# Optimization experiments

Measured on AMD Instinct MI355X. Metric: run time of the kernel, lower is better.

The kernel has to match this reference:

```python
import jax, jax.numpy as jnp
import numpy as np

BS, TS, NE, ED = 32, 64, 64, 96
E = 256        # attn_embed_dim
H = 4          # attn_n_heads
HD = E // H    # head dim
RNN_H = 256
N_ACT = 32
NA = 16        # n_agents


def setup_inputs():
    key = jax.random.key(0)
    ks = jax.random.split(key, 40)
    entities = jax.random.normal(ks[0], (BS, TS, NE, ED), jnp.float32)
    obs_mask = jax.random.randint(ks[1], (BS, TS, NE, NE), 0, 2).astype(jnp.float32)  # 1 = masked
    entity_mask = (jax.random.uniform(ks[2], (BS, TS, NE)) < 0.1).astype(jnp.float32)  # 1 = inactive
    hidden_state = jnp.zeros((BS * NA, RNN_H), jnp.float32)
    it = iter(range(3, 40))
    def lin(fi, fo):
        return jax.random.normal(ks[next(it)], (fi, fo), jnp.float32) / np.sqrt(fi).astype(np.float32)
    p = dict(
        fc1_w=lin(ED, E), fc1_b=jnp.zeros((E,), jnp.float32),
        attn_in_w=lin(E, 3 * E), attn_out_w=lin(E, E), attn_out_b=jnp.zeros((E,), jnp.float32),
        fc2_w=lin(2 * E, RNN_H), fc2_b=jnp.zeros((RNN_H,), jnp.float32),
        gru_w_ih=lin(RNN_H, 3 * RNN_H), gru_w_hh=lin(RNN_H, 3 * RNN_H),
        gru_b_ih=jnp.zeros((3 * RNN_H,), jnp.float32), gru_b_hh=jnp.zeros((3 * RNN_H,), jnp.float32),
        fc3_w=lin(RNN_H, N_ACT), fc3_b=jnp.zeros((N_ACT,), jnp.float32),
        fcmsg1_w=lin(ED, E), fcmsg1_b=jnp.zeros((E,), jnp.float32),
        lmsg_in_w=lin(E, 3 * E), lmsg_out_w=lin(E, E), lmsg_out_b=jnp.zeros((E,), jnp.float32),
        gmsg_in_w=lin(E, 3 * E), gmsg_out_w=lin(E, E), gmsg_out_b=jnp.zeros((E,), jnp.float32),
        gate_in_w=lin(E, 3 * E), gate_out_w=lin(E, E), gate_out_b=jnp.zeros((E,), jnp.float32),
        gatefc1_w=lin(ED, E), gatefc1_b=jnp.zeros((E,), jnp.float32),
        gatefc2_w=lin(E, 2), gatefc2_b=jnp.zeros((2,), jnp.float32),
    )
    return dict(entities=entities, obs_mask=obs_mask, entity_mask=entity_mask,
                hidden_state=hidden_state, **p)


def _attn(x, in_w, out_w, out_b, pre_mask, post_mask):
    """REFIL EntityAttentionLayer: n_queries = NA agent rows, masks use 1 = masked."""
    B, ne, e = x.shape
    q, k, v = jnp.split(x @ in_w, 3, axis=-1)                       # each [B, ne, E]
    q = q[:, :NA].reshape(B, NA, H, HD).transpose(0, 2, 1, 3)        # [B, H, NA, HD]
    k = k.reshape(B, ne, H, HD).transpose(0, 2, 1, 3)                # [B, H, ne, HD]
    v = v.reshape(B, ne, H, HD).transpose(0, 2, 1, 3)
    logits = jnp.einsum('bhqd,bhkd->bhqk', q, k) / jnp.asarray(np.sqrt(HD), x.dtype)
    m = pre_mask[:, None, :NA, :]                                    # [B, 1, NA, ne]
    logits = jnp.where(m > 0, jnp.asarray(-1e9, x.dtype), logits)
    # softmax; zeroing masked cols also reproduces torch's NaN->0 for fully-masked rows
    w = jax.nn.softmax(logits, axis=-1) * (1.0 - m)
    out = jnp.einsum('bhqk,bhkd->bhqd', w, v).transpose(0, 2, 1, 3).reshape(B, NA, e)
    out = out @ out_w + out_b
    return out * (1.0 - post_mask[..., None])                        # masked_fill(post_mask, 0)


def _forward(entities, obs_mask, entity_mask, hidden_state,
             fc1_w, fc1_b, attn_in_w, attn_out_w, attn_out_b, fc2_w, fc2_b,
             gru_w_ih, gru_w_hh, gru_b_ih, gru_b_hh, fc3_w, fc3_b,
             fcmsg1_w, fcmsg1_b, lmsg_in_w, lmsg_out_w, lmsg_out_b,
             gmsg_in_w, gmsg_out_w, gmsg_out_b, gate_in_w, gate_out_w, gate_out_b,
             gatefc1_w, gatefc1_b, gatefc2_w, gatefc2_b):
    bs, ts, ne, ed = entities.shape
    B = bs * ts
    ent = entities.reshape(B, ne, ed)
    om = obs_mask.reshape(B, ne, ne)
    em = entity_mask.reshape(B, ne)
    agent_mask = em[:, :NA]                                          # [B, NA]
    full_obs_mask = 1.0 - (1.0 - agent_mask[:, None, :]) * (1.0 - agent_mask[:, :, None])

    x1 = jax.nn.relu(ent @ fc1_w + fc1_b)
    x2 = _attn(x1, attn_in_w, attn_out_w, attn_out_b, om, agent_mask)          # [B, NA, E]

    x1_msg = jax.nn.relu(ent @ fcmsg1_w + fcmsg1_b)
    x1_gate = jax.nn.relu(ent @ gatefc1_w + gatefc1_b)
    x2_msg = _attn(x1_msg, lmsg_in_w, lmsg_out_w, lmsg_out_b, om, agent_mask)  # [B, NA, E]
    x2_gate = _attn(x1_gate, gate_in_w, gate_out_w, gate_out_b, om, agent_mask)
    x2_gate = x2_gate @ gatefc2_w + gatefc2_b                                   # [B, NA, 2]

    # argmax of softmax == argmax of logits; gate in {0,1}, non-differentiable
    gate = jnp.argmax(x2_gate, axis=-1).astype(entities.dtype)
    gated_msg = x2_msg * gate[..., None]
    global_msg = _attn(gated_msg, gmsg_in_w, gmsg_out_w, gmsg_out_b,
                       full_obs_mask, agent_mask)                               # [B, NA, E]

    x3 = jax.nn.relu(jnp.concatenate([x2, global_msg], axis=-1) @ fc2_w + fc2_b)
    x3 = x3.reshape(bs, ts, NA, RNN_H)

    # GRU recurrence over ts via scan; hidden flattened to [bs*NA, RNN_H]
    h0 = hidden_state.reshape(-1, RNN_H)
    xs = x3.transpose(1, 0, 2, 3).reshape(ts, bs * NA, RNN_H)

    def step(h, x):
        gi = x @ gru_w_ih + gru_b_ih
        gh = h @ gru_w_hh + gru_b_hh
        ir, iz, inn = jnp.split(gi, 3, axis=-1)
        hr, hz, hn = jnp.split(gh, 3, axis=-1)
        r = jax.nn.sigmoid(ir + hr)
        z = jax.nn.sigmoid(iz + hz)
        n = jnp.tanh(inn + r * hn)
        h_new = (1.0 - z) * n + z * h
        return h_new, h_new

    _, hs = jax.lax.scan(step, h0, xs)                               # [ts, bs*NA, RNN_H]
    hs = hs.reshape(ts, bs, NA, RNN_H).transpose(1, 0, 2, 3)         # [bs, ts, NA, RNN_H]

    q = hs @ fc3_w + fc3_b                                           # [bs, ts, NA, N_ACT]
    am = agent_mask.reshape(bs, ts, NA, 1)
    q = q * (1.0 - am)                                               # masked_fill(agent_mask, 0)
    return q, hs, x2_gate


def reference(entities, obs_mask, entity_mask, hidden_state,
              fc1_w, fc1_b, attn_in_w, attn_out_w, attn_out_b, fc2_w, fc2_b,
              gru_w_ih, gru_w_hh, gru_b_ih, gru_b_hh, fc3_w, fc3_b,
              fcmsg1_w, fcmsg1_b, lmsg_in_w, lmsg_out_w, lmsg_out_b,
              gmsg_in_w, gmsg_out_w, gmsg_out_b, gate_in_w, gate_out_w, gate_out_b,
              gatefc1_w, gatefc1_b, gatefc2_w, gatefc2_b):
    return _forward(entities, obs_mask, entity_mask, hidden_state,
                    fc1_w, fc1_b, attn_in_w, attn_out_w, attn_out_b, fc2_w, fc2_b,
                    gru_w_ih, gru_w_hh, gru_b_ih, gru_b_hh, fc3_w, fc3_b,
                    fcmsg1_w, fcmsg1_b, lmsg_in_w, lmsg_out_w, lmsg_out_b,
                    gmsg_in_w, gmsg_out_w, gmsg_out_b, gate_in_w, gate_out_w, gate_out_b,
                    gatefc1_w, gatefc1_b, gatefc2_w, gatefc2_b)
```

## Files before the change

kernel.cpp:

```cpp
#include <hip/hip_runtime.h>


#define DEV __device__ __forceinline__

typedef _Float16 f16x8 __attribute__((ext_vector_type(8)));
typedef _Float16 f16x4 __attribute__((ext_vector_type(4)));
typedef float    f32x4 __attribute__((ext_vector_type(4)));
typedef float    f32x16 __attribute__((ext_vector_type(16)));

DEV f32x4 mfma16(f16x8 a, f16x8 b, f32x4 c){
  return __builtin_amdgcn_mfma_f32_16x16x32_f16(a, b, c, 0, 0, 0);
}
DEV f32x16 mfma32(f16x8 a, f16x8 b, f32x16 c){
  return __builtin_amdgcn_mfma_f32_32x32x16_f16(a, b, c, 0, 0, 0);
}

template<int MODE> struct AB {
  f16x8 hi, lo;
  DEV void mf(const AB& b, f32x4& c) const {
    if constexpr (MODE){
      c = mfma16(lo, b.hi, c);
      c = mfma16(hi, b.lo, c);
    }
    c = mfma16(hi, b.hi, c);
  }
};

template<int MODE> DEV AB<MODE> ldW(const _Float16* p, int losz){
  AB<MODE> r; r.hi = *(const f16x8*)p;
  if constexpr (MODE) r.lo = *(const f16x8*)(p + losz);
  return r;
}
template<int MODE> DEV AB<MODE> ldL(const _Float16* ph, const _Float16* pl){
  AB<MODE> r; r.hi = *(const f16x8*)ph;
  if constexpr (MODE) r.lo = *(const f16x8*)pl;
  return r;
}
template<int MODE> DEV AB<MODE> ldF(const float* p){
  AB<MODE> r;
  f32x4 v0 = *(const f32x4*)p, v1 = *(const f32x4*)(p + 4);
#pragma unroll
  for (int i = 0; i < 4; ++i){
    float a = v0[i], b = v1[i];
    _Float16 ah = (_Float16)a, bh = (_Float16)b;
    r.hi[i] = ah; r.hi[i+4] = bh;
    if constexpr (MODE){
      r.lo[i]   = (_Float16)(a - (float)ah);
      r.lo[i+4] = (_Float16)(b - (float)bh);
    }
  }
  return r;
}
template<int MODE> DEV void stL(_Float16* ph, _Float16* pl, int idx, float v){
  _Float16 h = (_Float16)v;
  ph[idx] = h;
  if constexpr (MODE) pl[idx] = (_Float16)(v - (float)h);
}

struct WJobs {
  const float* src[15];
  unsigned off[15];
  int K[15], N[15], mode[15];
};

__global__ __launch_bounds__(256) void k0_conv(WJobs jb, char* ws){
  const int job = blockIdx.y;
  const int K = jb.K[job], N = jb.N[job];
  const int total = K * N;
  _Float16* dh = (_Float16*)(ws + jb.off[job]);
  const float* src = jb.src[job];
  const int m = jb.mode[job];
  for (int idx = blockIdx.x*256 + threadIdx.x; idx < total; idx += gridDim.x*256){
    int n = idx / K, k = idx - n*K;
    float v = src[(size_t)k*N + n];
    _Float16 h = (_Float16)v;
    dh[idx] = h;
    if (m) dh[total + idx] = (_Float16)(v - (float)h);
  }
}

__global__ __launch_bounds__(256) void k0w_gate(
    const float* __restrict__ Wout, const float* __restrict__ Wg2,
    const float* __restrict__ bo,   const float* __restrict__ Win,
    _Float16* __restrict__ wveff, float* __restrict__ beff)
{
  __shared__ float weff_s[256*2];
  const int tid = threadIdx.x;
  {
    float a0 = 0.f, a1 = 0.f;
    const float* wr = Wout + (size_t)tid*256;
    for (int f = 0; f < 256; ++f){ float x = wr[f]; a0 += x*Wg2[2*f]; a1 += x*Wg2[2*f+1]; }
    weff_s[tid*2] = a0; weff_s[tid*2+1] = a1;
  }
  if (tid < 2){
    float s = 0.f;
    for (int f = 0; f < 256; ++f) s += bo[f]*Wg2[2*f + tid];
    beff[tid] = s;
  }
  __syncthreads();
  {
    const int j = tid;
    for (int n = 0; n < 16; ++n){
      float v = 0.f;
      if (n < 8){
        int h = n >> 1, c = n & 1;
        const float* wr = Win + (size_t)j*768 + 512 + h*64;
        const float* we = weff_s + (h*64)*2 + c;
        for (int d = 0; d < 64; ++d) v += wr[d]*we[2*d];
      }
      _Float16 hi = (_Float16)v;
      wveff[n*256 + j] = hi;
      wveff[16*256 + n*256 + j] = (_Float16)(v - (float)hi);
    }
  }
}

__global__ __launch_bounds__(512) void k1_all(
    const float* __restrict__ ent, const float* __restrict__ om, const float* __restrict__ em,
    const _Float16* __restrict__ W1a, const float* __restrict__ b1a,
    const _Float16* __restrict__ WINa,
    const _Float16* __restrict__ WOUTa, const float* __restrict__ boa,
    float* __restrict__ x2outa,
    const _Float16* __restrict__ W1b, const float* __restrict__ b1b,
    const _Float16* __restrict__ WINb,
    const _Float16* __restrict__ WOUTb, const float* __restrict__ bob,
    float* __restrict__ x2outb,
    const _Float16* __restrict__ W1g, const float* __restrict__ b1g,
    const _Float16* __restrict__ WINg,
    const _Float16* __restrict__ WVEFF,
    const float* __restrict__ beff, const float* __restrict__ gb2,
    float* __restrict__ og, float* __restrict__ gate)
{
  const int tid = threadIdx.x;
  const int w = tid >> 6, lg = (tid >> 4) & 3, li = tid & 15;
  extern __shared__ char smem[];

  if (blockIdx.x < 2048){
    const int br = blockIdx.x >> 10;
    const int p  = blockIdx.x & 1023;
    const int bb2[2] = { 2*p, 2*p + 1 };
    const _Float16* W1   = br ? W1b   : W1a;
    const float*    b1   = br ? b1b   : b1a;
    const _Float16* WIN  = br ? WINb  : WINa;
    const _Float16* WOUT = br ? WOUTb : WOUTa;
    const float*    bo   = br ? bob   : boa;
    float*          x2out= br ? x2outb: x2outa;

    const int wi = w & 3, ih = w >> 2;
    const int l = tid & 63;
    const int r32 = l & 31, kh = (l >> 5)*8;

    _Float16* x1   = (_Float16*)smem;
    _Float16* Ks   = (_Float16*)(smem + 67584);
    _Float16* Vs   = (_Float16*)(smem + 86016);
    _Float16* Qful = (_Float16*)(smem + 104448);
    float*    lgs  = (float*)(smem + 121344);
    _Float16* Ps   = (_Float16*)(smem + 130560);
    _Float16* outp = (_Float16*)(smem + 135168);

    {
      const int b = bb2[ih];
      _Float16* x1p = x1 + ih*16896;
      const int mt = wi & 1, ntb = (wi >> 1)*4;
      f32x16 acc0 = 0.f, acc1 = 0.f, acc2 = 0.f, acc3 = 0.f;
#pragma unroll
      for (int kk = 0; kk < 6; ++kk){
        AB<0> a = ldF<0>(ent + ((size_t)b*64 + mt*32 + r32)*96 + kk*16 + kh);
        f16x8 B0 = *(const f16x8*)(W1 + (size_t)((ntb + 0)*32 + r32)*96 + kk*16 + kh);
        f16x8 B1 = *(const f16x8*)(W1 + (size_t)((ntb + 1)*32 + r32)*96 + kk*16 + kh);
        f16x8 B2 = *(const f16x8*)(W1 + (size_t)((ntb + 2)*32 + r32)*96 + kk*16 + kh);
        f16x8 B3 = *(const f16x8*)(W1 + (size_t)((ntb + 3)*32 + r32)*96 + kk*16 + kh);
        acc0 = mfma32(a.hi, B0, acc0);
        acc1 = mfma32(a.hi, B1, acc1);
        acc2 = mfma32(a.hi, B2, acc2);
        acc3 = mfma32(a.hi, B3, acc3);
      }
#pragma unroll
      for (int s = 0; s < 4; ++s){
        const f32x16& ac = (s == 0) ? acc0 : (s == 1) ? acc1 : (s == 2) ? acc2 : acc3;
        int col = (ntb + s)*32 + r32;
        float bias = b1[col];
#pragma unroll
        for (int reg = 0; reg < 16; ++reg){
          int row = (reg & 3) + 8*(reg >> 2) + 4*(l >> 5);
          x1p[(mt*32 + row)*264 + col] = (_Float16)fmaxf(ac[reg] + bias, 0.f);
        }
      }
    }
    __syncthreads();

    {
      f32x16 acc = 0.f;
      const int itq = r32 >> 4, qr = r32 & 15;
      for (int kk = 0; kk < 16; ++kk){
        f16x8 A = *(const f16x8*)(x1 + itq*16896 + qr*264 + kk*16 + kh);
        f16x8 B = *(const f16x8*)(WIN + (size_t)(w*32 + r32)*256 + kk*16 + kh);
        acc = mfma32(A, B, acc);
      }
#pragma unroll
      for (int reg = 0; reg < 16; ++reg){
        int row = (reg & 3) + 8*(reg >> 2) + 4*(l >> 5);
        Qful[(row >> 4)*4224 + (row & 15)*264 + w*32 + r32] = (_Float16)acc[reg];
      }
    }
    __syncthreads();

    for (int h = 0; h < 4; ++h){
      if (w < 4){
        const int kt = w >> 1, dt = w & 1;
        f32x16 acc0 = 0.f, acc1 = 0.f;
        for (int kk = 0; kk < 16; ++kk){
          int ao = (kt*32 + r32)*264 + kk*16 + kh;
          f16x8 A0 = *(const f16x8*)(x1 + ao);
          f16x8 A1 = *(const f16x8*)(x1 + 16896 + ao);
          f16x8 B = *(const f16x8*)(WIN + (size_t)(256 + 64*h + dt*32 + r32)*256 + kk*16 + kh);
          acc0 = mfma32(A0, B, acc0);
          acc1 = mfma32(A1, B, acc1);
        }
#pragma unroll
        for (int reg = 0; reg < 16; ++reg){
          int row = (reg & 3) + 8*(reg >> 2) + 4*(l >> 5);
          Ks[(kt*32 + row)*72 + dt*32 + r32]        = (_Float16)acc0[reg];
          Ks[4608 + (kt*32 + row)*72 + dt*32 + r32] = (_Float16)acc1[reg];
        }
      } else {
        const int wv = w - 4;
        const int kt = wv >> 1, dt = wv & 1;
        f32x16 acc0 = 0.f, acc1 = 0.f;
        for (int kk = 0; kk < 16; ++kk){
          int ao = (kt*32 + r32)*264 + kk*16 + kh;
          f16x8 A0 = *(const f16x8*)(x1 + ao);
          f16x8 A1 = *(const f16x8*)(x1 + 16896 + ao);
          f16x8 B = *(const f16x8*)(WIN + (size_t)(512 + 64*h + dt*32 + r32)*256 + kk*16 + kh);
          acc0 = mfma32(A0, B, acc0);
          acc1 = mfma32(A1, B, acc1);
        }
#pragma unroll
        for (int rr = 0; rr < 4; ++rr){
          f16x4 p0, p1;
#pragma unroll
          for (int q4 = 0; q4 < 4; ++q4){
            p0[q4] = (_Float16)acc0[rr*4 + q4];
            p1[q4] = (_Float16)acc1[rr*4 + q4];
          }
          int key = kt*32 + rr*8 + 4*(l >> 5);
          *(f16x4*)(Vs + (dt*32 + r32)*72 + key)        = p0;
          *(f16x4*)(Vs + 4608 + (dt*32 + r32)*72 + key) = p1;
        }
      }
      __syncthreads();
      {
        const int b = bb2[ih];
        f32x4 acc = 0.f;
#pragma unroll
        for (int kk = 0; kk < 2; ++kk){
          f16x8 A = *(const f16x8*)(Qful + ih*4224 + li*264 + 64*h + kk*32 + lg*8);
          f16x8 B = *(const f16x8*)(Ks + ih*4608 + (16*wi + li)*72 + kk*32 + lg*8);
          acc = mfma16(A, B, acc);
        }
#pragma unroll
        for (int j = 0; j < 4; ++j){
          int q = 4*lg + j, key = 16*wi + li;
          float v = acc[j] * 0.125f;
          float m = om[((size_t)b*64 + q)*64 + key];
          if (m > 0.f) v = -1e9f;
          lgs[ih*1152 + q*72 + key] = v;
        }
      }
      __syncthreads();
      {
        const int it = tid >> 8, q = (tid >> 4) & 15, i16 = tid & 15;
        const int b = bb2[it];
        float pv[4], mx = -3e38f;
#pragma unroll
        for (int u = 0; u < 4; ++u){ pv[u] = lgs[it*1152 + q*72 + i16 + 16*u]; mx = fmaxf(mx, pv[u]); }
#pragma unroll
        for (int d = 1; d < 16; d <<= 1) mx = fmaxf(mx, __shfl_xor(mx, d, 16));
        float s = 0.f;
#pragma unroll
        for (int u = 0; u < 4; ++u){ pv[u] = expf(pv[u] - mx); s += pv[u]; }
#pragma unroll
        for (int d = 1; d < 16; d <<= 1) s += __shfl_xor(s, d, 16);
#pragma unroll
        for (int u = 0; u < 4; ++u){
          int key = i16 + 16*u;
          float m = om[((size_t)b*64 + q)*64 + key];
          Ps[it*1152 + q*72 + key] = (_Float16)((pv[u]/s)*(1.f - m));
        }
      }
      __syncthreads();
      {
        f32x4 acc = 0.f;
#pragma unroll
        for (int kk = 0; kk < 2; ++kk){
          f16x8 A = *(const f16x8*)(Ps + ih*1152 + li*72 + kk*32 + lg*8);
          f16x8 B = *(const f16x8*)(Vs + ih*4608 + (16*wi + li)*72 + kk*32 + lg*8);
          acc = mfma16(A, B, acc);
        }
#pragma unroll
        for (int j = 0; j < 4; ++j)
          outp[ih*4224 + (4*lg + j)*264 + 64*h + 16*wi + li] = (_Float16)acc[j];
      }
      __syncthreads();
    }

    {
      f32x16 acc = 0.f;
      const int ito = r32 >> 4, qr = r32 & 15;
      for (int kk = 0; kk < 16; ++kk){
        f16x8 A = *(const f16x8*)(outp + ito*4224 + qr*264 + kk*16 + kh);
        f16x8 B = *(const f16x8*)(WOUT + (size_t)(w*32 + r32)*256 + kk*16 + kh);
        acc = mfma32(A, B, acc);
      }
      int col = w*32 + r32;
      float bias = bo[col];
#pragma unroll
      for (int reg = 0; reg < 16; ++reg){
        int row = (reg & 3) + 8*(reg >> 2) + 4*(l >> 5);
        int it2 = row >> 4, q2 = row & 15;
        const int b = bb2[it2];
        float v = (acc[reg] + bias) * (1.f - em[(size_t)b*64 + q2]);
        x2out[((size_t)b*16 + q2)*256 + col] = v;
      }
    }
    return;
  }

  {
    constexpr int W1SZ = 96*256, WINSZ = 256*768, WVSZ = 16*256;
    const int b = blockIdx.x - 2048;
    const int l = tid & 63;
    const int r32 = l & 31, kh = (l >> 5)*8;

    char* sp = smem;
    _Float16* x1h = (_Float16*)sp; sp += 64*264*2;
    _Float16* x1l = (_Float16*)sp; sp += 64*264*2;
    _Float16* Kh  = (_Float16*)sp; sp += 64*72*2;
    _Float16* Kl  = (_Float16*)sp; sp += 64*72*2;
    _Float16* Qh  = (_Float16*)sp; sp += 16*264*2;
    _Float16* Ql  = (_Float16*)sp; sp += 16*264*2;
    float*    lgs = (float*)sp;    sp += 16*72*4;
    float*    Ps  = (float*)sp;    sp += 16*66*4;
    float*    v2s = (float*)sp;    sp += 64*18*4;
    float*  ogacc = (float*)sp;    sp += 32*4;
    float*  Kpart = (float*)sp;    sp += 8192*4;

    {
      const int mt = w & 1, ntb = (w >> 1)*2;
      f32x16 acc0 = 0.f, acc1 = 0.f;
#pragma unroll
      for (int kk = 0; kk < 6; ++kk){
        AB<1> a = ldF<1>(ent + ((size_t)b*64 + mt*32 + r32)*96 + kk*16 + kh);
#pragma unroll
        for (int s = 0; s < 2; ++s){
          const _Float16* bp = W1g + (size_t)((ntb + s)*32 + r32)*96 + kk*16 + kh;
          f16x8 Bh = *(const f16x8*)bp;
          f16x8 Bl = *(const f16x8*)(bp + W1SZ);
          f32x16& ac = s ? acc1 : acc0;
          ac = mfma32(a.lo, Bh, ac);
          ac = mfma32(a.hi, Bl, ac);
          ac = mfma32(a.hi, Bh, ac);
        }
      }
#pragma unroll
      for (int s = 0; s < 2; ++s){
        const f32x16& ac = s ? acc1 : acc0;
        int col = (ntb + s)*32 + r32;
        float bias = b1g[col];
#pragma unroll
        for (int reg = 0; reg < 16; ++reg){
          int row = (reg & 3) + 8*(reg >> 2) + 4*(l >> 5);
          stL<1>(x1h, x1l, (mt*32 + row)*264 + col, fmaxf(ac[reg] + bias, 0.f));
        }
      }
    }
    if (tid < 32) ogacc[tid] = 0.f;
    __syncthreads();

    {
#pragma unroll
      for (int s = 0; s < 2; ++s){
        int nt = w + s*8;
        f32x4 acc = 0.f;
        for (int kk = 0; kk < 8; ++kk){
          int ao = li*264 + kk*32 + lg*8;
          AB<1> a = ldL<1>(x1h + ao, x1l + ao);
          AB<1> bb = ldW<1>(WINg + (size_t)(nt*16 + li)*256 + kk*32 + lg*8, WINSZ);
          a.mf(bb, acc);
        }
#pragma unroll
        for (int j = 0; j < 4; ++j)
          stL<1>(Qh, Ql, (4*lg + j)*264 + nt*16 + li, acc[j]);
      }
      if (w < 4){
        f32x4 acc = 0.f;
        for (int kk = 0; kk < 8; ++kk){
          int ao = (w*16 + li)*264 + kk*32 + lg*8;
          AB<1> a = ldL<1>(x1h + ao, x1l + ao);
          AB<1> bb = ldW<1>(WVEFF + (size_t)li*256 + kk*32 + lg*8, WVSZ);
          a.mf(bb, acc);
        }
#pragma unroll
        for (int j = 0; j < 4; ++j)
          v2s[(w*16 + 4*lg + j)*18 + li] = acc[j];
      }
    }
    __syncthreads();

    for (int h = 0; h < 4; ++h){
      {
        const int t = w & 3, kt = t >> 1, dt = t & 1, khalf = w >> 2;
        f32x16 acc = 0.f;
#pragma unroll
        for (int k8 = 0; k8 < 8; ++k8){
          int ko = (khalf*8 + k8)*16 + kh;
          int ao = (kt*32 + r32)*264 + ko;
          f16x8 ah = *(const f16x8*)(x1h + ao);
          f16x8 al = *(const f16x8*)(x1l + ao);
          const _Float16* bp = WINg + (size_t)(256 + h*64 + dt*32 + r32)*256 + ko;
          f16x8 Bh = *(const f16x8*)bp;
          f16x8 Bl = *(const f16x8*)(bp + WINSZ);
          acc = mfma32(al, Bh, acc);
          acc = mfma32(ah, Bl, acc);
          acc = mfma32(ah, Bh, acc);
        }
#pragma unroll
        for (int reg = 0; reg < 16; ++reg){
          int row = (reg & 3) + 8*(reg >> 2) + 4*(l >> 5);
          Kpart[((khalf*4 + t)*32 + row)*32 + r32] = acc[reg];
        }
      }
      __syncthreads();
      {
        for (int e = tid; e < 4096; e += 512){
          float s2 = Kpart[e] + Kpart[4096 + e];
          int t2 = e >> 10, idx = e & 1023, row = idx >> 5, col = idx & 31;
          stL<1>(Kh, Kl, ((t2 >> 1)*32 + row)*72 + (t2 & 1)*32 + col, s2);
        }
      }
      __syncthreads();
      if (w < 4){
        f32x4 acc = 0.f;
#pragma unroll
        for (int kk = 0; kk < 2; ++kk){
          int ao = li*264 + h*64 + kk*32 + lg*8;
          AB<1> a = ldL<1>(Qh + ao, Ql + ao);
          int bo_ = (16*w + li)*72 + kk*32 + lg*8;
          AB<1> bb = ldL<1>(Kh + bo_, Kl + bo_);
          a.mf(bb, acc);
        }
#pragma unroll
        for (int j = 0; j < 4; ++j){
          int q = 4*lg + j, key = 16*w + li;
          float v = acc[j] * 0.125f;
          float m = om[((size_t)b*64 + q)*64 + key];
          if (m > 0.f) v = -1e9f;
          lgs[q*72 + key] = v;
        }
      }
      __syncthreads();
      if (tid < 256){
        int q = tid >> 4, i16 = tid & 15;
        float pv[4], mx = -3e38f;
#pragma unroll
        for (int u = 0; u < 4; ++u){ pv[u] = lgs[q*72 + i16 + 16*u]; mx = fmaxf(mx, pv[u]); }
#pragma unroll
        for (int d = 1; d < 16; d <<= 1) mx = fmaxf(mx, __shfl_xor(mx, d, 16));
        float s = 0.f;
#pragma unroll
        for (int u = 0; u < 4; ++u){ pv[u] = expf(pv[u] - mx); s += pv[u]; }
#pragma unroll
        for (int d = 1; d < 16; d <<= 1) s += __shfl_xor(s, d, 16);
#pragma unroll
        for (int u = 0; u < 4; ++u){
          int key = i16 + 16*u;
          float m = om[((size_t)b*64 + q)*64 + key];
          Ps[q*66 + key] = (pv[u]/s)*(1.f - m);
        }
      }
      __syncthreads();
      if (tid < 256){
        int q = tid >> 4, l16 = tid & 15;
        float a0 = 0.f, a1 = 0.f;
#pragma unroll
        for (int u = 0; u < 4; ++u){
          int k = l16 + 16*u;
          float p2 = Ps[q*66 + k];
          a0 += p2 * v2s[k*18 + h*2];
          a1 += p2 * v2s[k*18 + h*2 + 1];
        }
#pragma unroll
        for (int d = 1; d < 16; d <<= 1){ a0 += __shfl_xor(a0, d, 16); a1 += __shfl_xor(a1, d, 16); }
        if (l16 == 0){ ogacc[q*2] += a0; ogacc[q*2 + 1] += a1; }
      }
      __syncthreads();
    }
    if (tid < 16){
      int q = tid;
      float am = em[(size_t)b*64 + q];
      float g0 = (1.f - am)*(ogacc[2*q]     + beff[0]) + gb2[0];
      float g1 = (1.f - am)*(ogacc[2*q + 1] + beff[1]) + gb2[1];
      og[((size_t)b*16 + q)*2]     = g0;
      og[((size_t)b*16 + q)*2 + 1] = g1;
      gate[(size_t)b*16 + q] = (g1 > g0) ? 1.f : 0.f;
    }
  }
}

__global__ __launch_bounds__(256) void k2_global(
    const float* __restrict__ em,
    const float* __restrict__ x2, const float* __restrict__ x2m,
    const float* __restrict__ gate,
    const _Float16* __restrict__ GMIN, const _Float16* __restrict__ GMOUT, const float* __restrict__ gob,
    const _Float16* __restrict__ FC2T, const float* __restrict__ fc2b,
    const _Float16* __restrict__ GIHT, const float* __restrict__ gib,
    float* __restrict__ gi)
{
  const int p = blockIdx.x;
  const int tid = threadIdx.x;
  const int w = tid >> 6, lg = (tid >> 4) & 3, li = tid & 15;

  extern __shared__ char smem[];
  float*    gate_s = (float*)smem;
  _Float16* gm_s   = (_Float16*)(smem + 128);
  _Float16* Q2     = (_Float16*)(smem + 17024);
  _Float16* K2s    = (_Float16*)(smem + 21632);
  _Float16* Vt2    = (_Float16*)(smem + 26240);
  float*    lg2    = (float*)(smem + 36480);
  _Float16* P2     = (_Float16*)(smem + 39552);
  _Float16* outp   = (_Float16*)(smem + 42112);
  _Float16* cat_s  = (_Float16*)(smem + 59008);
  _Float16* x3_s   = (_Float16*)(smem + 92288);

  if (tid < 32){
    int it = tid >> 4, q = tid & 15;
    gate_s[it*16 + q] = gate[(size_t)(2*p + it)*16 + q];
  }
  __syncthreads();
#pragma unroll
  for (int it = 0; it < 2; ++it){
    const int b = 2*p + it;
    for (int idx = tid; idx < 4096; idx += 256){
      int q = idx >> 8, d = idx & 255;
      gm_s[it*4224 + q*264 + d]  = (_Float16)(x2m[((size_t)b*16 + q)*256 + d] * gate_s[it*16 + q]);
      cat_s[it*8320 + q*520 + d] = (_Float16)(x2[((size_t)b*16 + q)*256 + d]);
    }
  }
  for (int idx = tid; idx < 2*64*40; idx += 256) Vt2[idx] = (_Float16)0.f;
  for (int idx = tid; idx < 2*16*40; idx += 256) P2[idx] = (_Float16)0.f;
  __syncthreads();
  for (int h = 0; h < 4; ++h){
    {
      f32x4 aq0 = 0.f, aq1 = 0.f, ak0 = 0.f, ak1 = 0.f, av0 = 0.f, av1 = 0.f;
      for (int kk = 0; kk < 8; ++kk){
        f16x8 A0 = *(const f16x8*)(gm_s + li*264 + kk*32 + lg*8);
        f16x8 A1 = *(const f16x8*)(gm_s + 4224 + li*264 + kk*32 + lg*8);
        f16x8 Bq = *(const f16x8*)(GMIN + (size_t)(      64*h + 16*w + li)*256 + kk*32 + lg*8);
        f16x8 Bk = *(const f16x8*)(GMIN + (size_t)(256 + 64*h + 16*w + li)*256 + kk*32 + lg*8);
        f16x8 Bv = *(const f16x8*)(GMIN + (size_t)(512 + 64*h + 16*w + li)*256 + kk*32 + lg*8);
        aq0 = mfma16(A0, Bq, aq0); aq1 = mfma16(A1, Bq, aq1);
        ak0 = mfma16(A0, Bk, ak0); ak1 = mfma16(A1, Bk, ak1);
        av0 = mfma16(A0, Bv, av0); av1 = mfma16(A1, Bv, av1);
      }
#pragma unroll
      for (int j = 0; j < 4; ++j){
        int rw = 4*lg + j, dim = 16*w + li;
        Q2[rw*72 + dim]         = (_Float16)aq0[j];
        Q2[1152 + rw*72 + dim]  = (_Float16)aq1[j];
        K2s[rw*72 + dim]        = (_Float16)ak0[j];
        K2s[1152 + rw*72 + dim] = (_Float16)ak1[j];
        Vt2[dim*40 + rw]        = (_Float16)av0[j];
        Vt2[2560 + dim*40 + rw] = (_Float16)av1[j];
      }
    }
    __syncthreads();
    if (w < 2){
      const int it = w, b = 2*p + it;
      f32x4 acc = 0.f;
#pragma unroll
      for (int kk = 0; kk < 2; ++kk){
        f16x8 A = *(const f16x8*)(Q2  + it*1152 + li*72 + kk*32 + lg*8);
        f16x8 B = *(const f16x8*)(K2s + it*1152 + li*72 + kk*32 + lg*8);
        acc = mfma16(A, B, acc);
      }
      float amk = em[(size_t)b*64 + li];
#pragma unroll
      for (int j = 0; j < 4; ++j){
        int q = 4*lg + j;
        float amq = em[(size_t)b*64 + q];
        float m = 1.f - (1.f - amq)*(1.f - amk);
        float v = acc[j]*0.125f;
        if (m > 0.f) v = -1e9f;
        lg2[it*384 + q*24 + li] = v;
      }
    }
    __syncthreads();
    {
      int q = tid >> 4, key = tid & 15;
#pragma unroll
      for (int it = 0; it < 2; ++it){
        const int b = 2*p + it;
        float v = lg2[it*384 + q*24 + key];
        float mx = v;
#pragma unroll
        for (int d = 1; d < 16; d <<= 1) mx = fmaxf(mx, __shfl_xor(mx, d, 16));
        float pe = expf(v - mx);
        float s = pe;
#pragma unroll
        for (int d = 1; d < 16; d <<= 1) s += __shfl_xor(s, d, 16);
        float amq = em[(size_t)b*64 + q], amk = em[(size_t)b*64 + key];
        float m = 1.f - (1.f - amq)*(1.f - amk);
        P2[it*640 + q*40 + key] = (_Float16)((pe/s)*(1.f - m));
      }
    }
    __syncthreads();
    {
#pragma unroll
      for (int it = 0; it < 2; ++it){
        f32x4 acc = 0.f;
        f16x8 A = *(const f16x8*)(P2 + it*640 + li*40 + lg*8);
        f16x8 B = *(const f16x8*)(Vt2 + it*2560 + (16*w + li)*40 + lg*8);
        acc = mfma16(A, B, acc);
#pragma unroll
        for (int j = 0; j < 4; ++j)
          outp[it*4224 + (4*lg + j)*264 + 64*h + 16*w + li] = (_Float16)acc[j];
      }
    }
    __syncthreads();
  }
  {
#pragma unroll
    for (int c = 0; c < 4; ++c){
      int col = 64*w + 16*c + li;
      f32x4 a0 = 0.f, a1 = 0.f;
      for (int kk = 0; kk < 8; ++kk){
        f16x8 B  = *(const f16x8*)(GMOUT + (size_t)col*256 + kk*32 + lg*8);
        f16x8 A0 = *(const f16x8*)(outp + li*264 + kk*32 + lg*8);
        f16x8 A1 = *(const f16x8*)(outp + 4224 + li*264 + kk*32 + lg*8);
        a0 = mfma16(A0, B, a0);
        a1 = mfma16(A1, B, a1);
      }
      float bias = gob[col];
#pragma unroll
      for (int j = 0; j < 4; ++j){
        int q = 4*lg + j;
        float m0 = 1.f - em[(size_t)(2*p)*64 + q];
        float m1 = 1.f - em[(size_t)(2*p + 1)*64 + q];
        cat_s[q*520 + 256 + col]        = (_Float16)((a0[j] + bias)*m0);
        cat_s[8320 + q*520 + 256 + col] = (_Float16)((a1[j] + bias)*m1);
      }
    }
  }
  __syncthreads();
  {
#pragma unroll
    for (int c = 0; c < 4; ++c){
      int col = 64*w + 16*c + li;
      f32x4 a0 = 0.f, a1 = 0.f;
      for (int kk = 0; kk < 16; ++kk){
        f16x8 B  = *(const f16x8*)(FC2T + (size_t)col*512 + kk*32 + lg*8);
        f16x8 A0 = *(const f16x8*)(cat_s + li*520 + kk*32 + lg*8);
        f16x8 A1 = *(const f16x8*)(cat_s + 8320 + li*520 + kk*32 + lg*8);
        a0 = mfma16(A0, B, a0);
        a1 = mfma16(A1, B, a1);
      }
      float bias = fc2b[col];
#pragma unroll
      for (int j = 0; j < 4; ++j){
        x3_s[(4*lg + j)*264 + col]        = (_Float16)fmaxf(a0[j] + bias, 0.f);
        x3_s[4224 + (4*lg + j)*264 + col] = (_Float16)fmaxf(a1[j] + bias, 0.f);
      }
    }
  }
  __syncthreads();
  {
    const int r0 = ((2*p) >> 6)*16, t0 = (2*p) & 63;
#pragma unroll
    for (int cc = 0; cc < 12; ++cc){
      int col = (w*12 + cc)*16 + li;
      f32x4 a0 = 0.f, a1 = 0.f;
      for (int kk = 0; kk < 8; ++kk){
        f16x8 B  = *(const f16x8*)(GIHT + (size_t)col*256 + kk*32 + lg*8);
        f16x8 A0 = *(const f16x8*)(x3_s + li*264 + kk*32 + lg*8);
        f16x8 A1 = *(const f16x8*)(x3_s + 4224 + li*264 + kk*32 + lg*8);
        a0 = mfma16(A0, B, a0);
        a1 = mfma16(A1, B, a1);
      }
      float bias = gib[col];
#pragma unroll
      for (int j = 0; j < 4; ++j){
        int q = 4*lg + j;
        gi[((size_t)((r0 + q)*64 + t0))*768 + col]     = a0[j] + bias;
        gi[((size_t)((r0 + q)*64 + t0 + 1))*768 + col] = a1[j] + bias;
      }
    }
  }
}

__global__ __launch_bounds__(256) void k3_gru(
    const _Float16* __restrict__ WHH, const float* __restrict__ bhh,
    const float* __restrict__ gi, const float* __restrict__ h0,
    float* __restrict__ hs)
{
  const int rb = blockIdx.x;
  const int row0 = rb * 16;
  const int tid = threadIdx.x;
  const int w = tid >> 6, lg = (tid >> 4) & 3, li = tid & 15;

  extern __shared__ char smem3[];
  _Float16* hf16 = (_Float16*)smem3;
  float* hf32 = (float*)(smem3 + 8448);
  float* gh   = (float*)(smem3 + 8448 + 16640);
  float* bhs  = (float*)(smem3 + 8448 + 16640 + 49664);

  for (int idx = tid; idx < 768; idx += 256) bhs[idx] = bhh[idx];
  for (int idx = tid; idx < 4096; idx += 256){
    int r = idx >> 8, d = idx & 255;
    float v = h0[(size_t)(row0 + r)*256 + d];
    hf32[r*260 + d] = v;
    hf16[r*264 + d] = (_Float16)v;
  }
  __syncthreads();

  const int er = tid >> 4;
  const int d0 = (tid & 15) * 16;

  for (int t = 0; t < 64; ++t){
    const float* gp = gi + ((size_t)(row0 + er)*64 + t)*768 + d0;
    f32x4 gr[4], gz[4], gn[4];
#pragma unroll
    for (int v = 0; v < 4; ++v){
      gr[v] = *(const f32x4*)(gp + v*4);
      gz[v] = *(const f32x4*)(gp + 256 + v*4);
      gn[v] = *(const f32x4*)(gp + 512 + v*4);
    }
    f16x8 a[8];
#pragma unroll
    for (int kk = 0; kk < 8; ++kk)
      a[kk] = *(const f16x8*)(hf16 + li*264 + kk*32 + lg*8);
    f32x4 acc[12];
#pragma unroll
    for (int c = 0; c < 12; ++c) acc[c] = 0.f;
#pragma unroll
    for (int c = 0; c < 12; ++c){
      const _Float16* bp = WHH + (size_t)(w*192 + c*16 + li)*256 + lg*8;
#pragma unroll
      for (int kk = 0; kk < 8; ++kk)
        acc[c] = mfma16(a[kk], *(const f16x8*)(bp + kk*32), acc[c]);
    }
#pragma unroll
    for (int c = 0; c < 12; ++c){
      int col = w*192 + c*16 + li;
#pragma unroll
      for (int j = 0; j < 4; ++j)
        gh[(4*lg + j)*776 + col] = acc[c][j];
    }
    __syncthreads();
    {
      float* hp32 = hf32 + er*260 + d0;
      float* hsp  = hs + ((size_t)(rb*64 + t)*16 + er)*256 + d0;
      f16x8 hv8[2];
#pragma unroll
      for (int v = 0; v < 4; ++v){
        f32x4 xr = *(const f32x4*)(gh + er*776 +       d0 + v*4);
        f32x4 xz = *(const f32x4*)(gh + er*776 + 256 + d0 + v*4);
        f32x4 xn = *(const f32x4*)(gh + er*776 + 512 + d0 + v*4);
        f32x4 hold = *(const f32x4*)(hp32 + v*4);
        f32x4 hout;
#pragma unroll
        for (int e = 0; e < 4; ++e){
          int d = d0 + v*4 + e;
          float rr_ = 1.f/(1.f + __expf(-(gr[v][e] + xr[e] + bhs[d])));
          float zz  = 1.f/(1.f + __expf(-(gz[v][e] + xz[e] + bhs[256 + d])));
          float pre = gn[v][e] + rr_*(xn[e] + bhs[512 + d]);
          float nn  = 1.f - 2.f/(1.f + __expf(2.f*pre));
          float hv = (1.f - zz)*nn + zz*hold[e];
          hout[e] = hv;
          int sl = v*4 + e;
          hv8[sl >> 3][sl & 7] = (_Float16)hv;
        }
        *(f32x4*)(hp32 + v*4) = hout;
        *(f32x4*)(hsp + v*4)  = hout;
      }
      *(f16x8*)(hf16 + er*264 + d0)     = hv8[0];
      *(f16x8*)(hf16 + er*264 + d0 + 8) = hv8[1];
    }
    __syncthreads();
  }
}

__global__ __launch_bounds__(256) void k4_q(
    const _Float16* __restrict__ FC3T, const float* __restrict__ fc3b,
    const float* __restrict__ em, const float* __restrict__ hs, float* __restrict__ qo)
{
  const int tid = threadIdx.x;
  const int w = tid >> 6, lg = (tid >> 4) & 3, li = tid & 15;
  const int rb = blockIdx.x*64 + 16*w;
  f32x4 acc[2];
#pragma unroll
  for (int c = 0; c < 2; ++c) acc[c] = 0.f;
  for (int kk = 0; kk < 8; ++kk){
    const float* ap = hs + (size_t)(rb + li)*256 + kk*32 + lg*8;
    f32x4 v0 = *(const f32x4*)ap, v1 = *(const f32x4*)(ap + 4);
    f16x8 A;
#pragma unroll
    for (int e = 0; e < 4; ++e){ A[e] = (_Float16)v0[e]; A[e+4] = (_Float16)v1[e]; }
#pragma unroll
    for (int c = 0; c < 2; ++c){
      f16x8 B = *(const f16x8*)(FC3T + (size_t)(16*c + li)*256 + kk*32 + lg*8);
      acc[c] = mfma16(A, B, acc[c]);
    }
  }
#pragma unroll
  for (int c = 0; c < 2; ++c){
    int col = 16*c + li;
    float bias = fc3b[col];
#pragma unroll
    for (int j = 0; j < 4; ++j){
      int row = rb + 4*lg + j;
      float am = em[(size_t)(row >> 4)*64 + (row & 15)];
      qo[(size_t)row*32 + col] = (acc[c][j] + bias)*(1.f - am);
    }
  }
}

extern "C" void kernel_launch(void* const* d_in, const int* in_sizes, int n_in,
                              void* d_out, int out_size, void* d_ws, size_t ws_size,
                              hipStream_t stream)
{
  constexpr size_t OFF_FC1T   = 0;
  constexpr size_t OFF_MSG1T  = 49152;
  constexpr size_t OFF_AINT   = 98304;
  constexpr size_t OFF_LINT   = 491520;
  constexpr size_t OFF_AOUTT  = 884736;
  constexpr size_t OFF_LOUTT  = 1015808;
  constexpr size_t OFF_GMINT  = 1146880;
  constexpr size_t OFF_GMOUTT = 1540096;
  constexpr size_t OFF_FC2T   = 1671168;
  constexpr size_t OFF_GIHT   = 1933312;
  constexpr size_t OFF_GHHT   = 2326528;
  constexpr size_t OFF_FC3T   = 2719744;
  constexpr size_t OFF_G1T    = 2736128;
  constexpr size_t OFF_GINT   = 2834432;
  constexpr size_t OFF_WVEFF  = 3620864;
  constexpr size_t OFF_BEFF   = 3637248;
  constexpr size_t OFF_GATE   = 3637504;
  constexpr size_t OFF_X2     = 3768576;
  constexpr size_t OFF_X2M    = 37323008;
  constexpr size_t OFF_GI     = 70877440;
  constexpr size_t NEED       = 171540736;
  if (ws_size < NEED) return;

  char* ws = (char*)d_ws;
  const float* ent = (const float*)d_in[0];
  const float* om  = (const float*)d_in[1];
  const float* em  = (const float*)d_in[2];

  WJobs jb{};
  int nj = 0;
  auto addj = [&](int src_idx, size_t off, int K, int N, int m){
    jb.src[nj] = (const float*)d_in[src_idx]; jb.off[nj] = (unsigned)off;
    jb.K[nj] = K; jb.N[nj] = N; jb.mode[nj] = m; ++nj;
  };
  addj(4,  OFF_FC1T,   96, 256, 0);
  addj(17, OFF_MSG1T,  96, 256, 0);
  addj(6,  OFF_AINT,  256, 768, 0);
  addj(19, OFF_LINT,  256, 768, 0);
  addj(7,  OFF_AOUTT, 256, 256, 0);
  addj(20, OFF_LOUTT, 256, 256, 0);
  addj(22, OFF_GMINT, 256, 768, 0);
  addj(23, OFF_GMOUTT,256, 256, 0);
  addj(9,  OFF_FC2T,  512, 256, 0);
  addj(11, OFF_GIHT,  256, 768, 0);
  addj(12, OFF_GHHT,  256, 768, 0);
  addj(15, OFF_FC3T,  256,  32, 0);
  addj(28, OFF_G1T,    96, 256, 1);
  addj(25, OFF_GINT,  256, 768, 1);
  k0_conv<<<dim3(96, nj), 256, 0, stream>>>(jb, ws);

  k0w_gate<<<1, 256, 0, stream>>>(
      (const float*)d_in[26], (const float*)d_in[30],
      (const float*)d_in[27], (const float*)d_in[25],
      (_Float16*)(ws + OFF_WVEFF), (float*)(ws + OFF_BEFF));

  constexpr int SMB = 156672, SMK2 = 109184, SM3 = 77824;
  (void)hipFuncSetAttribute(reinterpret_cast<const void*>(&k1_all),
                            hipFuncAttributeMaxDynamicSharedMemorySize, SMB);
  (void)hipFuncSetAttribute(reinterpret_cast<const void*>(&k2_global),
                            hipFuncAttributeMaxDynamicSharedMemorySize, SMK2);
  (void)hipFuncSetAttribute(reinterpret_cast<const void*>(&k3_gru),
                            hipFuncAttributeMaxDynamicSharedMemorySize, SM3);

  float* qout = (float*)d_out;
  float* hsout = qout + 1048576;
  float* gout = qout + 9437184;

  k1_all<<<4096, 512, SMB, stream>>>(ent, om, em,
      (const _Float16*)(ws + OFF_FC1T),  (const float*)d_in[5],
      (const _Float16*)(ws + OFF_AINT),
      (const _Float16*)(ws + OFF_AOUTT), (const float*)d_in[8],
      (float*)(ws + OFF_X2),
      (const _Float16*)(ws + OFF_MSG1T), (const float*)d_in[18],
      (const _Float16*)(ws + OFF_LINT),
      (const _Float16*)(ws + OFF_LOUTT), (const float*)d_in[21],
      (float*)(ws + OFF_X2M),
      (const _Float16*)(ws + OFF_G1T),   (const float*)d_in[29],
      (const _Float16*)(ws + OFF_GINT),
      (const _Float16*)(ws + OFF_WVEFF),
      (const float*)(ws + OFF_BEFF), (const float*)d_in[31],
      gout, (float*)(ws + OFF_GATE));

  k2_global<<<1024, 256, SMK2, stream>>>(em,
      (const float*)(ws + OFF_X2), (const float*)(ws + OFF_X2M),
      (const float*)(ws + OFF_GATE),
      (const _Float16*)(ws + OFF_GMINT), (const _Float16*)(ws + OFF_GMOUTT), (const float*)d_in[24],
      (const _Float16*)(ws + OFF_FC2T), (const float*)d_in[10],
      (const _Float16*)(ws + OFF_GIHT), (const float*)d_in[13],
      (float*)(ws + OFF_GI));

  k3_gru<<<32, 256, SM3, stream>>>(
      (const _Float16*)(ws + OFF_GHHT), (const float*)d_in[14],
      (const float*)(ws + OFF_GI), (const float*)d_in[3], hsout);

  k4_q<<<512, 256, 0, stream>>>(
      (const _Float16*)(ws + OFF_FC3T), (const float*)d_in[16],
      em, hsout, qout);
}
```

Before: 1.312 ms.

## Use 32x32 MFMA tiles in k2 GEMMs and double GRU block threads

The three dense GEMM stages in k2_global (gmsg out-projection, fc2, GRU input projection) now use 32x32x16 MFMA over both time steps at once, instead of paired 16x16x32 MFMAs per time step. Each B fragment now covers 32 rows, which is meant to cut the number of MFMA issues and weight reloads. The sequential GRU kernel k3 now runs 512 threads per block, so each wave handles half the columns and each thread half the elements. This shortens the serial per-step critical path. In exchange, k2 does more scattered shared-memory writes in its epilogue and k3 has more waves taking part in each barrier.

After: 1.154 ms. -12.0%, faster.

```diff
diff --git a/kernel.cpp b/kernel.cpp
--- a/kernel.cpp
+++ b/kernel.cpp
@@ -519,6 +519,8 @@
   const int p = blockIdx.x;
   const int tid = threadIdx.x;
   const int w = tid >> 6, lg = (tid >> 4) & 3, li = tid & 15;
+  const int l = tid & 63;
+  const int r32 = l & 31, kh = (l >> 5)*8;
 
   extern __shared__ char smem[];
   float*    gate_s = (float*)smem;
@@ -629,75 +631,75 @@
     __syncthreads();
   }
   {
-#pragma unroll
-    for (int c = 0; c < 4; ++c){
-      int col = 64*w + 16*c + li;
-      f32x4 a0 = 0.f, a1 = 0.f;
-      for (int kk = 0; kk < 8; ++kk){
-        f16x8 B  = *(const f16x8*)(GMOUT + (size_t)col*256 + kk*32 + lg*8);
-        f16x8 A0 = *(const f16x8*)(outp + li*264 + kk*32 + lg*8);
-        f16x8 A1 = *(const f16x8*)(outp + 4224 + li*264 + kk*32 + lg*8);
-        a0 = mfma16(A0, B, a0);
-        a1 = mfma16(A1, B, a1);
-      }
+    const int ito = r32 >> 4, qr = r32 & 15;
+#pragma unroll
+    for (int s = 0; s < 2; ++s){
+      int nt = 2*w + s;
+      f32x16 acc = 0.f;
+      for (int kk = 0; kk < 16; ++kk){
+        f16x8 A = *(const f16x8*)(outp + ito*4224 + qr*264 + kk*16 + kh);
+        f16x8 B = *(const f16x8*)(GMOUT + (size_t)(nt*32 + r32)*256 + kk*16 + kh);
+        acc = mfma32(A, B, acc);
+      }
+      int col = nt*32 + r32;
       float bias = gob[col];
 #pragma unroll
-      for (int j = 0; j < 4; ++j){
-        int q = 4*lg + j;
-        float m0 = 1.f - em[(size_t)(2*p)*64 + q];
-        float m1 = 1.f - em[(size_t)(2*p + 1)*64 + q];
-        cat_s[q*520 + 256 + col]        = (_Float16)((a0[j] + bias)*m0);
-        cat_s[8320 + q*520 + 256 + col] = (_Float16)((a1[j] + bias)*m1);
+      for (int reg = 0; reg < 16; ++reg){
+        int row = (reg & 3) + 8*(reg >> 2) + 4*(l >> 5);
+        int it2 = row >> 4, q2 = row & 15;
+        float m = 1.f - em[(size_t)(2*p + it2)*64 + q2];
+        cat_s[it2*8320 + q2*520 + 256 + col] = (_Float16)((acc[reg] + bias)*m);
       }
     }
   }
   __syncthreads();
   {
-#pragma unroll
-    for (int c = 0; c < 4; ++c){
-      int col = 64*w + 16*c + li;
-      f32x4 a0 = 0.f, a1 = 0.f;
-      for (int kk = 0; kk < 16; ++kk){
-        f16x8 B  = *(const f16x8*)(FC2T + (size_t)col*512 + kk*32 + lg*8);
-        f16x8 A0 = *(const f16x8*)(cat_s + li*520 + kk*32 + lg*8);
-        f16x8 A1 = *(const f16x8*)(cat_s + 8320 + li*520 + kk*32 + lg*8);
-        a0 = mfma16(A0, B, a0);
-        a1 = mfma16(A1, B, a1);
-      }
+    const int ito = r32 >> 4, qr = r32 & 15;
+#pragma unroll
+    for (int s = 0; s < 2; ++s){
+      int nt = 2*w + s;
+      f32x16 acc = 0.f;
+      for (int kk = 0; kk < 32; ++kk){
+        f16x8 A = *(const f16x8*)(cat_s + ito*8320 + qr*520 + kk*16 + kh);
+        f16x8 B = *(const f16x8*)(FC2T + (size_t)(nt*32 + r32)*512 + kk*16 + kh);
+        acc = mfma32(A, B, acc);
+      }
+      int col = nt*32 + r32;
       float bias = fc2b[col];
 #pragma unroll
-      for (int j = 0; j < 4; ++j){
-        x3_s[(4*lg + j)*264 + col]        = (_Float16)fmaxf(a0[j] + bias, 0.f);
-        x3_s[4224 + (4*lg + j)*264 + col] = (_Float16)fmaxf(a1[j] + bias, 0.f);
+      for (int reg = 0; reg < 16; ++reg){
+        int row = (reg & 3) + 8*(reg >> 2) + 4*(l >> 5);
+        int it2 = row >> 4, q2 = row & 15;
+        x3_s[it2*4224 + q2*264 + col] = (_Float16)fmaxf(acc[reg] + bias, 0.f);
       }
     }
   }
   __syncthreads();
   {
     const int r0 = ((2*p) >> 6)*16, t0 = (2*p) & 63;
-#pragma unroll
-    for (int cc = 0; cc < 12; ++cc){
-      int col = (w*12 + cc)*16 + li;
-      f32x4 a0 = 0.f, a1 = 0.f;
-      for (int kk = 0; kk < 8; ++kk){
-        f16x8 B  = *(const f16x8*)(GIHT + (size_t)col*256 + kk*32 + lg*8);
-        f16x8 A0 = *(const f16x8*)(x3_s + li*264 + kk*32 + lg*8);
-        f16x8 A1 = *(const f16x8*)(x3_s + 4224 + li*264 + kk*32 + lg*8);
-        a0 = mfma16(A0, B, a0);
-        a1 = mfma16(A1, B, a1);
-      }
+    const int ito = r32 >> 4, qr = r32 & 15;
+#pragma unroll
+    for (int s = 0; s < 6; ++s){
+      int nt = 6*w + s;
+      f32x16 acc = 0.f;
+      for (int kk = 0; kk < 16; ++kk){
+        f16x8 A = *(const f16x8*)(x3_s + ito*4224 + qr*264 + kk*16 + kh);
+        f16x8 B = *(const f16x8*)(GIHT + (size_t)(nt*32 + r32)*256 + kk*16 + kh);
+        acc = mfma32(A, B, acc);
+      }
+      int col = nt*32 + r32;
       float bias = gib[col];
 #pragma unroll
-      for (int j = 0; j < 4; ++j){
-        int q = 4*lg + j;
-        gi[((size_t)((r0 + q)*64 + t0))*768 + col]     = a0[j] + bias;
-        gi[((size_t)((r0 + q)*64 + t0 + 1))*768 + col] = a1[j] + bias;
-      }
-    }
-  }
-}
-
-__global__ __launch_bounds__(256) void k3_gru(
+      for (int reg = 0; reg < 16; ++reg){
+        int row = (reg & 3) + 8*(reg >> 2) + 4*(l >> 5);
+        int it2 = row >> 4, q2 = row & 15;
+        gi[((size_t)((r0 + q2)*64 + t0 + it2))*768 + col] = acc[reg] + bias;
+      }
+    }
+  }
+}
+
+__global__ __launch_bounds__(512) void k3_gru(
     const _Float16* __restrict__ WHH, const float* __restrict__ bhh,
     const float* __restrict__ gi, const float* __restrict__ h0,
     float* __restrict__ hs)
@@ -713,8 +715,8 @@
   float* gh   = (float*)(smem3 + 8448 + 16640);
   float* bhs  = (float*)(smem3 + 8448 + 16640 + 49664);
 
-  for (int idx = tid; idx < 768; idx += 256) bhs[idx] = bhh[idx];
-  for (int idx = tid; idx < 4096; idx += 256){
+  for (int idx = tid; idx < 768; idx += 512) bhs[idx] = bhh[idx];
+  for (int idx = tid; idx < 4096; idx += 512){
     int r = idx >> 8, d = idx & 255;
     float v = h0[(size_t)(row0 + r)*256 + d];
     hf32[r*260 + d] = v;
@@ -722,14 +724,14 @@
   }
   __syncthreads();
 
-  const int er = tid >> 4;
-  const int d0 = (tid & 15) * 16;
+  const int er = tid >> 5;
+  const int dd = (tid & 31) * 8;
 
   for (int t = 0; t < 64; ++t){
-    const float* gp = gi + ((size_t)(row0 + er)*64 + t)*768 + d0;
-    f32x4 gr[4], gz[4], gn[4];
-#pragma unroll
-    for (int v = 0; v < 4; ++v){
+    const float* gp = gi + ((size_t)(row0 + er)*64 + t)*768 + dd;
+    f32x4 gr[2], gz[2], gn[2];
+#pragma unroll
+    for (int v = 0; v < 2; ++v){
       gr[v] = *(const f32x4*)(gp + v*4);
       gz[v] = *(const f32x4*)(gp + 256 + v*4);
       gn[v] = *(const f32x4*)(gp + 512 + v*4);
@@ -738,52 +740,50 @@
 #pragma unroll
     for (int kk = 0; kk < 8; ++kk)
       a[kk] = *(const f16x8*)(hf16 + li*264 + kk*32 + lg*8);
-    f32x4 acc[12];
-#pragma unroll
-    for (int c = 0; c < 12; ++c) acc[c] = 0.f;
-#pragma unroll
-    for (int c = 0; c < 12; ++c){
-      const _Float16* bp = WHH + (size_t)(w*192 + c*16 + li)*256 + lg*8;
+    f32x4 acc[6];
+#pragma unroll
+    for (int c = 0; c < 6; ++c) acc[c] = 0.f;
+#pragma unroll
+    for (int c = 0; c < 6; ++c){
+      const _Float16* bp = WHH + (size_t)(w*96 + c*16 + li)*256 + lg*8;
 #pragma unroll
       for (int kk = 0; kk < 8; ++kk)
         acc[c] = mfma16(a[kk], *(const f16x8*)(bp + kk*32), acc[c]);
     }
 #pragma unroll
-    for (int c = 0; c < 12; ++c){
-      int col = w*192 + c*16 + li;
+    for (int c = 0; c < 6; ++c){
+      int col = w*96 + c*16 + li;
 #pragma unroll
       for (int j = 0; j < 4; ++j)
         gh[(4*lg + j)*776 + col] = acc[c][j];
     }
     __syncthreads();
     {
-      float* hp32 = hf32 + er*260 + d0;
-      float* hsp  = hs + ((size_t)(rb*64 + t)*16 + er)*256 + d0;
-      f16x8 hv8[2];
-#pragma unroll
-      for (int v = 0; v < 4; ++v){
-        f32x4 xr = *(const f32x4*)(gh + er*776 +       d0 + v*4);
-        f32x4 xz = *(const f32x4*)(gh + er*776 + 256 + d0 + v*4);
-        f32x4 xn = *(const f32x4*)(gh + er*776 + 512 + d0 + v*4);
+      float* hp32 = hf32 + er*260 + dd;
+      float* hsp  = hs + ((size_t)(rb*64 + t)*16 + er)*256 + dd;
+      f16x8 hv8;
+#pragma unroll
+      for (int v = 0; v < 2; ++v){
+        f32x4 xr = *(const f32x4*)(gh + er*776 +       dd + v*4);
+        f32x4 xz = *(const f32x4*)(gh + er*776 + 256 + dd + v*4);
+        f32x4 xn = *(const f32x4*)(gh + er*776 + 512 + dd + v*4);
         f32x4 hold = *(const f32x4*)(hp32 + v*4);
         f32x4 hout;
 #pragma unroll
         for (int e = 0; e < 4; ++e){
-          int d = d0 + v*4 + e;
+          int d = dd + v*4 + e;
           float rr_ = 1.f/(1.f + __expf(-(gr[v][e] + xr[e] + bhs[d])));
           float zz  = 1.f/(1.f + __expf(-(gz[v][e] + xz[e] + bhs[256 + d])));
           float pre = gn[v][e] + rr_*(xn[e] + bhs[512 + d]);
           float nn  = 1.f - 2.f/(1.f + __expf(2.f*pre));
           float hv = (1.f - zz)*nn + zz*hold[e];
           hout[e] = hv;
-          int sl = v*4 + e;
-          hv8[sl >> 3][sl & 7] = (_Float16)hv;
+          hv8[v*4 + e] = (_Float16)hv;
         }
         *(f32x4*)(hp32 + v*4) = hout;
         *(f32x4*)(hsp + v*4)  = hout;
       }
-      *(f16x8*)(hf16 + er*264 + d0)     = hv8[0];
-      *(f16x8*)(hf16 + er*264 + d0 + 8) = hv8[1];
+      *(f16x8*)(hf16 + er*264 + dd) = hv8;
     }
     __syncthreads();
   }
@@ -918,7 +918,7 @@
       (const _Float16*)(ws + OFF_GIHT), (const float*)d_in[13],
       (float*)(ws + OFF_GI));
 
-  k3_gru<<<32, 256, SM3, stream>>>(
+  k3_gru<<<32, 512, SM3, stream>>>(
       (const _Float16*)(ws + OFF_GHHT), (const float*)d_in[14],
       (const float*)(ws + OFF_GI), (const float*)d_in[3], hsout);
 
```
